# Optimization experiments

Hardware: AMD Instinct MI355X
Metric: run time of the kernel (lower is better)

Reference implementation:

```python
import jax, jax.numpy as jnp
import numpy as np

B, L, D_IN, H, N, NL = 16, 5000, 12, 256, 32, 4  # N = d_state//2 complex modes


def layer_norm(x, g, b, eps=1e-5):
    m = x.mean(-1, keepdims=True)
    v = ((x - m) ** 2).mean(-1, keepdims=True)
    return (x - m) * jax.lax.rsqrt(v + eps) * g + b


def s4d_kernel(log_dt, logA_re, A_im, Cp, length):
    # S4D-style diagonal SSM kernel (ZOH discretization), conjugate-symmetric -> 2*real
    dt = jnp.exp(log_dt)                      # (H,)
    A = -jnp.exp(logA_re) + 1j * A_im         # (H, N)
    C = Cp[..., 0] + 1j * Cp[..., 1]          # (H, N)
    dtA = A * dt[:, None]                     # (H, N)
    Ct = C * (jnp.exp(dtA) - 1.0) / A         # (H, N)
    V = jnp.exp(dtA[:, :, None] * jnp.arange(length, dtype=log_dt.dtype))  # (H, N, L) Vandermonde
    return 2.0 * jnp.einsum('hn,hnl->hl', Ct, V).real  # (H, L)


def s4_block(u, log_dt, logA_re, A_im, Cp, D, W_glu, b_glu):
    # u: (B, L, H), transposed=False convention
    length = u.shape[1]
    K = s4d_kernel(log_dt, logA_re, A_im, Cp, length)     # (H, L)
    n_fft = 2 * length
    k_f = jnp.fft.rfft(K, n=n_fft)                        # (H, F)
    u_f = jnp.fft.rfft(u, n=n_fft, axis=1)                # (B, F, H)
    y = jnp.fft.irfft(u_f * k_f.T[None], n=n_fft, axis=1)[:, :length]  # causal conv
    y = y + u * D                                         # skip connection
    y = jax.nn.gelu(y)
    y = y @ W_glu + b_glu                                 # (B, L, 2H)
    return jax.nn.glu(y, axis=-1)                         # (B, L, H)


def setup_inputs() -> dict:
    key = jax.random.key(0)
    ks = jax.random.split(key, 8)
    dt_min, dt_max = 1e-3, 1e-1
    log_dt = np.log(dt_min) + jax.random.uniform(ks[2], (NL, H)) * (np.log(dt_max) - np.log(dt_min))
    A_im = jnp.broadcast_to(np.pi * jnp.arange(N, dtype=jnp.float32), (NL, H, N)).copy()
    return {
        'x': jax.random.normal(ks[0], (B, L, D_IN), jnp.float32),
        'W_in': jax.random.normal(ks[1], (D_IN, H), jnp.float32) / np.sqrt(D_IN),
        'b_in': jnp.zeros((H,), jnp.float32),
        'ln_g': jnp.ones((NL, H), jnp.float32),
        'ln_b': jnp.zeros((NL, H), jnp.float32),
        'log_dt': log_dt.astype(jnp.float32),
        'logA_re': jnp.full((NL, H, N), np.log(0.5), jnp.float32),
        'A_im': A_im,
        'Cp': jax.random.normal(ks[3], (NL, H, N, 2), jnp.float32) * (0.5 ** 0.5),
        'D': jax.random.normal(ks[4], (NL, H), jnp.float32),
        'W_glu': jax.random.normal(ks[5], (NL, H, 2 * H), jnp.float32) / np.sqrt(H),
        'b_glu': jnp.zeros((NL, 2 * H), jnp.float32),
        'fn_g': jnp.ones((H,), jnp.float32),
        'fn_b': jnp.zeros((H,), jnp.float32),
    }


def reference(x, W_in, b_in, ln_g, ln_b, log_dt, logA_re, A_im, Cp, D, W_glu, b_glu, fn_g, fn_b):
    x = x @ W_in + b_in  # (B, L, H)
    for i in range(NL):
        z = layer_norm(x, ln_g[i], ln_b[i])  # prenorm
        residual = z
        y = s4_block(z, log_dt[i], logA_re[i], A_im[i], Cp[i], D[i], W_glu[i], b_glu[i])
        x = y + residual  # dropout is identity in eval
    return layer_norm(x, fn_g, fn_b)
```

## Files before the change

### kernel.cpp

```cpp
#include <hip/hip_runtime.h>
#include <math.h>

#define BB 16
#define LL 5000
#define DIN 12
#define HH 256
#define NN 32
#define NLAYER 4
#define LC 128
#define NCH 40
#define TAIL 8
#define COLS (BB*NCH)
#define NROWS (BB*LL)
#define KU 192

typedef __attribute__((ext_vector_type(8))) _Float16 f16x8;
typedef __attribute__((ext_vector_type(4))) float f32x4;

__device__ __forceinline__ float fast_gelu(float a) {
  float z = fmaf(0.0713548163f * a, a * a, 1.5957691216f * a);
  float e = __expf(-z);
  return a * __builtin_amdgcn_rcpf(1.0f + e);
}

__device__ __forceinline__ unsigned pk2h(float a, float b) {
  union { _Float16 h[2]; unsigned u; } x;
  x.h[0] = (_Float16)a; x.h[1] = (_Float16)b;
  return x.u;
}

__device__ __forceinline__ float2 upk2(unsigned u) {
  union { unsigned u; _Float16 h[2]; } x;
  x.u = u;
  return make_float2((float)x.h[0], (float)x.h[1]);
}

__global__ __launch_bounds__(128) void paramT_kernel(
    const float* __restrict__ log_dt, const float* __restrict__ logA_re,
    const float* __restrict__ A_im, const float* __restrict__ Cp,
    const float* __restrict__ Dv, int l,
    _Float16* __restrict__ Tc, _Float16* __restrict__ V, float* __restrict__ WLc) {
  int h = blockIdx.x;
  int t = threadIdx.x;
  __shared__ float s_are[NN], s_aim[NN], s_cre[NN], s_cim[NN];
  __shared__ float s_K[128];
  if (t < NN) {
    int n = t;
    int idx = (l * HH + h) * NN + n;
    float dt = expf(log_dt[l * HH + h]);
    float Are = -expf(logA_re[idx]);
    float Aim = A_im[idx];
    float are = Are * dt, aim = Aim * dt;
    float e = expf(are);
    float wre = e * cosf(aim), wim = e * sinf(aim);
    float cr = Cp[2 * idx], ci = Cp[2 * idx + 1];
    float nre = wre - 1.0f, nim = wim;
    float tre = cr * nre - ci * nim;
    float tim = cr * nim + ci * nre;
    float inv = 1.0f / (Are * Are + Aim * Aim);
    s_are[n] = are; s_aim[n] = aim;
    s_cre[n] = 2.0f * (tre * Are + tim * Aim) * inv;
    s_cim[n] = 2.0f * (tim * Are - tre * Aim) * inv;
    float eL = expf(128.0f * are);
    float ang = 128.0f * aim;
    WLc[h * 64 + 2 * n] = eL * cosf(ang);
    WLc[h * 64 + 2 * n + 1] = eL * sinf(ang);
  }
  __syncthreads();
  {
    float ksum = 0.0f;
    unsigned* brow = (unsigned*)(Tc + ((size_t)h * 128 + t) * KU + 128);
    for (int n = 0; n < NN; n++) {
      float are = s_are[n], aim = s_aim[n];
      float cre = s_cre[n], cim = s_cim[n];
      float ft = (float)t;
      float E = expf(are * ft);
      float a = aim * ft;
      float wtre = E * cosf(a), wtim = E * sinf(a);
      ksum = fmaf(cre, wtre, ksum);
      ksum = fmaf(-cim, wtim, ksum);
      float ew = expf(are);
      float wre = ew * cosf(aim), wim = ew * sinf(aim);
      float wpre = wtre * wre - wtim * wim;
      float wpim = wtre * wim + wtim * wre;
      float bre = cre * wpre - cim * wpim;
      float bim = -(cre * wpim + cim * wpre);
      brow[n] = pk2h(bre, bim);
      float fk = (float)(127 - t);
      float E2 = expf(are * fk);
      float a2 = aim * fk;
      V[((size_t)h * 64 + 2 * n) * 128 + t] = (_Float16)(E2 * cosf(a2));
      V[((size_t)h * 64 + 2 * n + 1) * 128 + t] = (_Float16)(E2 * sinf(a2));
    }
    s_K[t] = ksum;
  }
  __syncthreads();
  float D = Dv[l * HH + h];
  unsigned* row = (unsigned*)(Tc + ((size_t)h * 128 + t) * KU);
  for (int q = 0; q < 64; q++) {
    float v0 = 0.0f, v1 = 0.0f;
    int d0 = t - 2 * q;
    int d1 = d0 - 1;
    if (d0 >= 0) v0 = s_K[d0] + (d0 == 0 ? D : 0.0f);
    if (d1 >= 0) v1 = s_K[d1] + (d1 == 0 ? D : 0.0f);
    row[q] = pk2h(v0, v1);
  }
}

__global__ __launch_bounds__(256) void wt_kernel(
    const float* __restrict__ W, _Float16* __restrict__ Wt) {
  int gid = blockIdx.x * 256 + threadIdx.x;
  int l = gid >> 9, col = gid & 511;
  const float* w = W + (size_t)l * HH * 512 + col;
  _Float16* o = Wt + (size_t)gid * HH;
  for (int k = 0; k < HH; k++) o[k] = (_Float16)(w[(size_t)k * 512]);
}

__global__ __launch_bounds__(256) void proj_kernel(
    const float* __restrict__ x, const float* __restrict__ Win,
    const float* __restrict__ bin, _Float16* __restrict__ X) {
  int tp = threadIdx.x & 127, rs = threadIdx.x >> 7;
  int h0 = 2 * tp;
  float w0[DIN], w1[DIN];
#pragma unroll
  for (int k = 0; k < DIN; k++) {
    w0[k] = Win[k * HH + h0];
    w1[k] = Win[k * HH + h0 + 1];
  }
  float b0 = bin[h0], b1 = bin[h0 + 1];
  for (int row = blockIdx.x * 2 + rs; row < NROWS; row += gridDim.x * 2) {
    float a0 = b0, a1 = b1;
#pragma unroll
    for (int k = 0; k < DIN; k++) {
      float xv = x[(size_t)row * DIN + k];
      a0 = fmaf(xv, w0[k], a0);
      a1 = fmaf(xv, w1[k], a1);
    }
    *(unsigned*)(X + (size_t)row * HH + h0) = pk2h(a0, a1);
  }
}

__global__ __launch_bounds__(256) void ln_kernel(
    const _Float16* __restrict__ in, float* __restrict__ out,
    const float* __restrict__ g, const float* __restrict__ b) {
  int wave = threadIdx.x >> 6, lane = threadIdx.x & 63;
  int row = blockIdx.x * 4 + wave;
  uint2 pv = *(const uint2*)(in + (size_t)row * HH + 4 * lane);
  float2 v01 = upk2(pv.x), v23 = upk2(pv.y);
  float s = v01.x + v01.y + v23.x + v23.y;
  float q = v01.x * v01.x + v01.y * v01.y + v23.x * v23.x + v23.y * v23.y;
#pragma unroll
  for (int m = 1; m < 64; m <<= 1) { s += __shfl_xor(s, m); q += __shfl_xor(q, m); }
  float mean = s * (1.0f / HH);
  float var = q * (1.0f / HH) - mean * mean;
  float rstd = rsqrtf(var + 1e-5f);
  float4 gg = ((const float4*)g)[lane];
  float4 bb = ((const float4*)b)[lane];
  float4 o;
  o.x = (v01.x - mean) * rstd * gg.x + bb.x;
  o.y = (v01.y - mean) * rstd * gg.y + bb.y;
  o.z = (v23.x - mean) * rstd * gg.z + bb.z;
  o.w = (v23.y - mean) * rstd * gg.w + bb.w;
  ((float4*)(out + (size_t)row * HH))[lane] = o;
}

__global__ __launch_bounds__(256) void lnU_kernel(
    _Float16* __restrict__ stream, _Float16* __restrict__ U,
    const float* __restrict__ g, const float* __restrict__ b) {
  __shared__ unsigned short Ut[128][260];
  int col = blockIdx.x;
  int bI = col / NCH, cI = col % NCH;
  int len = (cI == NCH - 1) ? TAIL : 128;
  int wave = threadIdx.x >> 6, lane = threadIdx.x & 63;
  if (len < 128) {
    for (int idx = threadIdx.x; idx < (128 - len) * 260; idx += 256) {
      int r = idx / 260;
      Ut[len + r][idx - r * 260] = 0;
    }
  }
  float4 gg = ((const float4*)g)[lane];
  float4 bv = ((const float4*)b)[lane];
  size_t base = ((size_t)bI * LL + (size_t)cI * 128) * HH;
  for (int it = 0; it < 32; it++) {
    int tau = it * 4 + wave;
    if (tau < len) {
      uint2 pv = *(const uint2*)(stream + base + (size_t)tau * HH + 4 * lane);
      float2 v01 = upk2(pv.x), v23 = upk2(pv.y);
      float s = v01.x + v01.y + v23.x + v23.y;
      float q = v01.x * v01.x + v01.y * v01.y + v23.x * v23.x + v23.y * v23.y;
#pragma unroll
      for (int m = 1; m < 64; m <<= 1) { s += __shfl_xor(s, m); q += __shfl_xor(q, m); }
      float mean = s * (1.0f / HH);
      float var = q * (1.0f / HH) - mean * mean;
      float rstd = rsqrtf(var + 1e-5f);
      float o0 = (v01.x - mean) * rstd * gg.x + bv.x;
      float o1 = (v01.y - mean) * rstd * gg.y + bv.y;
      float o2 = (v23.x - mean) * rstd * gg.z + bv.z;
      float o3 = (v23.y - mean) * rstd * gg.w + bv.w;
      uint2 p;
      p.x = pk2h(o0, o1);
      p.y = pk2h(o2, o3);
      *(uint2*)(stream + base + (size_t)tau * HH + 4 * lane) = p;
      *(uint2*)&Ut[tau][4 * lane] = p;
    }
  }
  __syncthreads();
  for (int rep = 0; rep < 8; rep++) {
    int linear = rep * 256 + threadIdx.x;
    int h = linear >> 3, ub = linear & 7;
    unsigned* dst = (unsigned*)(U + ((size_t)h * COLS + col) * KU);
#pragma unroll
    for (int s2 = 0; s2 < 8; s2++) {
      int u = ub + s2 * 8;
      unsigned val = (unsigned)Ut[2 * u][h] | ((unsigned)Ut[2 * u + 1][h] << 16);
      dst[u] = val;
    }
  }
}

__global__ __launch_bounds__(256) void gemmA_kernel(
    const _Float16* __restrict__ V, const _Float16* __restrict__ U,
    _Float16* __restrict__ P) {
  __shared__ _Float16 As[64 * 72];
  __shared__ _Float16 Bs[64 * 72];
  int h = blockIdx.x, c0 = blockIdx.y * 64;
  int t = threadIdx.x;
  int w = t >> 6, lane = t & 63, lr = lane & 15, quad = lane >> 4;
  int mh = w & 1, nh = w >> 1;
  f32x4 acc[2][2];
#pragma unroll
  for (int i = 0; i < 2; i++)
#pragma unroll
    for (int j = 0; j < 2; j++) acc[i][j] = (f32x4)(0.0f);

  for (int kt = 0; kt < 128; kt += 64) {
#pragma unroll
    for (int i = 0; i < 2; i++) {
      int idx = t + 256 * i;
      int m = idx >> 3, q = idx & 7;
      *(uint4*)&As[m * 72 + q * 8] =
          *(const uint4*)(V + ((size_t)h * 64 + m) * 128 + kt + q * 8);
      *(uint4*)&Bs[m * 72 + q * 8] =
          *(const uint4*)(U + ((size_t)h * COLS + c0 + m) * KU + kt + q * 8);
    }
    __syncthreads();
#pragma unroll
    for (int ks = 0; ks < 2; ks++) {
      f16x8 af[2], bf[2];
#pragma unroll
      for (int i = 0; i < 2; i++)
        af[i] = *(const f16x8*)&As[(mh * 32 + i * 16 + lr) * 72 + ks * 32 + quad * 8];
#pragma unroll
      for (int j = 0; j < 2; j++)
        bf[j] = *(const f16x8*)&Bs[(nh * 32 + j * 16 + lr) * 72 + ks * 32 + quad * 8];
#pragma unroll
      for (int i = 0; i < 2; i++)
#pragma unroll
        for (int j = 0; j < 2; j++)
          acc[i][j] = __builtin_amdgcn_mfma_f32_16x16x32_f16(af[i], bf[j], acc[i][j], 0, 0, 0);
    }
    __syncthreads();
  }
#pragma unroll
  for (int i = 0; i < 2; i++) {
#pragma unroll
    for (int j = 0; j < 2; j++) {
      int n2 = mh * 32 + i * 16 + quad * 4;
      int col = c0 + nh * 32 + j * 16 + lr;
      f32x4 a = acc[i][j];
      uint2 r;
      r.x = pk2h(a[0], a[1]);
      r.y = pk2h(a[2], a[3]);
      *(uint2*)(P + ((size_t)h * COLS + col) * 64 + n2) = r;
    }
  }
}

__global__ __launch_bounds__(256) void combine_kernel(
    const _Float16* __restrict__ P, _Float16* __restrict__ U,
    const float* __restrict__ WLc) {
  int h = blockIdx.x >> 1;
  int bh = blockIdx.x & 1;
  int n = threadIdx.x & 31;
  int b = bh * 8 + (threadIdx.x >> 5);
  float wre = WLc[h * 64 + 2 * n], wim = WLc[h * 64 + 2 * n + 1];
  const _Float16* p = P + ((size_t)h * COLS + (size_t)b * NCH) * 64 + 2 * n;
  _Float16* u = U + ((size_t)h * COLS + (size_t)b * NCH) * KU + 128 + 2 * n;
  float cre = 0.0f, cim = 0.0f;
#pragma unroll 4
  for (int c = 0; c < NCH; c++) {
    float2 v = upk2(*(const unsigned*)(p + (size_t)c * 64));
    *(unsigned*)(u + (size_t)c * KU) = pk2h(cre, cim);
    float nre = fmaf(wre, cre, v.x) - wim * cim;
    float nim = fmaf(wre, cim, v.y) + wim * cre;
    cre = nre; cim = nim;
  }
}

__global__ __launch_bounds__(256) void gemmC_kernel(
    const _Float16* __restrict__ Tc, const _Float16* __restrict__ U,
    _Float16* __restrict__ Yt) {
  __shared__ _Float16 As[128 * 72];
  __shared__ _Float16 Bs[64 * 72];
  int h = blockIdx.x, c0 = blockIdx.y * 64;
  int t = threadIdx.x;
  int w = t >> 6, lane = t & 63, lr = lane & 15, quad = lane >> 4;
  f32x4 acc[2][4];
#pragma unroll
  for (int i = 0; i < 2; i++)
#pragma unroll
    for (int j = 0; j < 4; j++) acc[i][j] = (f32x4)(0.0f);

  for (int kt = 0; kt < KU; kt += 64) {
#pragma unroll
    for (int i = 0; i < 4; i++) {
      int idx = t + 256 * i;
      int m = idx >> 3, q = idx & 7;
      *(uint4*)&As[m * 72 + q * 8] =
          *(const uint4*)(Tc + ((size_t)h * 128 + m) * KU + kt + q * 8);
    }
#pragma unroll
    for (int i = 0; i < 2; i++) {
      int idx = t + 256 * i;
      int jj = idx >> 3, q = idx & 7;
      *(uint4*)&Bs[jj * 72 + q * 8] =
          *(const uint4*)(U + ((size_t)h * COLS + c0 + jj) * KU + kt + q * 8);
    }
    __syncthreads();
#pragma unroll
    for (int ks = 0; ks < 2; ks++) {
      f16x8 af[2], bf[4];
#pragma unroll
      for (int i = 0; i < 2; i++)
        af[i] = *(const f16x8*)&As[(w * 32 + i * 16 + lr) * 72 + ks * 32 + quad * 8];
#pragma unroll
      for (int j = 0; j < 4; j++)
        bf[j] = *(const f16x8*)&Bs[(j * 16 + lr) * 72 + ks * 32 + quad * 8];
#pragma unroll
      for (int i = 0; i < 2; i++)
#pragma unroll
        for (int j = 0; j < 4; j++)
          acc[i][j] = __builtin_amdgcn_mfma_f32_16x16x32_f16(af[i], bf[j], acc[i][j], 0, 0, 0);
    }
    __syncthreads();
  }
#pragma unroll
  for (int i = 0; i < 2; i++) {
#pragma unroll
    for (int j = 0; j < 4; j++) {
      int tb = w * 32 + i * 16 + quad * 4;
      int col = c0 + j * 16 + lr;
      f32x4 a = acc[i][j];
      uint2 r;
      r.x = pk2h(fast_gelu(a[0]), fast_gelu(a[1]));
      r.y = pk2h(fast_gelu(a[2]), fast_gelu(a[3]));
      *(uint2*)(Yt + ((size_t)h * COLS + col) * 128 + tb) = r;
    }
  }
}

__global__ __launch_bounds__(256) void gemm_glu_mfma(
    const _Float16* __restrict__ Yt, const _Float16* __restrict__ Wt,
    const float* __restrict__ bg, _Float16* __restrict__ Xio) {
  __shared__ uint4 smemq[2304];
  _Float16* As = (_Float16*)smemq;
  _Float16* Bs = (_Float16*)smemq + 128 * 64;
  float* gl = (float*)smemq;
  int t = threadIdx.x;
  int col = blockIdx.x;
  int bI = col / NCH, pt = col % NCH;
  int len = (pt == NCH - 1) ? TAIL : 128;
  size_t row0 = (size_t)bI * LL + (size_t)pt * 128;
  int c0 = blockIdx.y * 64;
  int w = t >> 6, lane = t & 63;
  int lr = lane & 15, quad = lane >> 4;
  int rh = w & 1, ch = w >> 1;
  int oct = lane & 15, hq = lane >> 4;
  f32x4 acc[4][4];
#pragma unroll
  for (int i = 0; i < 4; i++)
#pragma unroll
    for (int j = 0; j < 4; j++) acc[i][j] = (f32x4)(0.0f);

  int jb[4] = {ch * 32, ch * 32 + 16, 64 + ch * 32, 80 + ch * 32};

  for (int kt = 0; kt < HH; kt += 64) {
#pragma unroll
    for (int p = 0; p < 4; p++) {
      int hl = p * 16 + w * 4 + hq;
      uint4 v = *(const uint4*)(Yt + ((size_t)(kt + hl) * COLS + col) * 128 + oct * 8);
      uint4 pv;
      pv.x = __shfl_xor((int)v.x, 16);
      pv.y = __shfl_xor((int)v.y, 16);
      pv.z = __shfl_xor((int)v.z, 16);
      pv.w = __shfl_xor((int)v.w, 16);
      if ((hq & 1) == 0) {
        const unsigned short* sv = (const unsigned short*)&v;
        const unsigned short* qv = (const unsigned short*)&pv;
        int h8 = hl >> 3;
        int hb2 = (hl & 7) * 2;
#pragma unroll
        for (int j = 0; j < 8; j++) {
          int tt = oct * 8 + j;
          int so = h8 ^ (tt & 7) ^ ((tt >> 3) & 7);
          *(unsigned*)((char*)As + tt * 128 + so * 16 + hb2) =
              (unsigned)sv[j] | ((unsigned)qv[j] << 16);
        }
      }
    }
#pragma unroll
    for (int i = 0; i < 4; i++) {
      int idx = t + 256 * i;
      int jj = idx >> 3, q = idx & 7;
      int colw = (jj < 64) ? (c0 + jj) : (192 + c0 + jj);
      *(uint4*)&Bs[jj * 72 + q * 8] =
          *(const uint4*)(Wt + (size_t)colw * HH + kt + q * 8);
    }
    __syncthreads();
#pragma unroll
    for (int ks = 0; ks < 2; ks++) {
      f16x8 af[4], bf[4];
#pragma unroll
      for (int i = 0; i < 4; i++) {
        int tt = rh * 64 + i * 16 + lr;
        int so = (ks * 4 + quad) ^ (tt & 7) ^ ((tt >> 3) & 7);
        af[i] = *(const f16x8*)((const char*)As + tt * 128 + so * 16);
      }
#pragma unroll
      for (int j = 0; j < 4; j++)
        bf[j] = *(const f16x8*)&Bs[(jb[j] + lr) * 72 + ks * 32 + quad * 8];
#pragma unroll
      for (int i = 0; i < 4; i++)
#pragma unroll
        for (int j = 0; j < 4; j++)
          acc[i][j] = __builtin_amdgcn_mfma_f32_16x16x32_f16(af[i], bf[j], acc[i][j], 0, 0, 0);
    }
    __syncthreads();
  }

#pragma unroll
  for (int i = 0; i < 4; i++) {
#pragma unroll
    for (int r = 0; r < 4; r++) {
      int rowl = rh * 64 + i * 16 + quad * 4 + r;
#pragma unroll
      for (int jp = 0; jp < 2; jp++) {
        int hl = ch * 32 + jp * 16 + lr;
        int h = c0 + hl;
        float g1 = acc[i][jp][r] + bg[h];
        float g2 = acc[i][jp + 2][r] + bg[256 + h];
        float sig = __builtin_amdgcn_rcpf(1.0f + __expf(-g2));
        gl[rowl * 68 + hl] = g1 * sig;
      }
    }
  }
  __syncthreads();

#pragma unroll
  for (int rep = 0; rep < 4; rep++) {
    int lin = rep * 256 + t;
    int rowl = lin >> 3, hc = lin & 7;
    if (rowl < len) {
      size_t row = row0 + rowl;
      int hb = c0 + hc * 8;
      uint4 zv = *(const uint4*)(Xio + row * HH + hb);
      float2 z01 = upk2(zv.x), z23 = upk2(zv.y), z45 = upk2(zv.z), z67 = upk2(zv.w);
      const float* gp = &gl[rowl * 68 + hc * 8];
      uint4 r;
      r.x = pk2h(gp[0] + z01.x, gp[1] + z01.y);
      r.y = pk2h(gp[2] + z23.x, gp[3] + z23.y);
      r.z = pk2h(gp[4] + z45.x, gp[5] + z45.y);
      r.w = pk2h(gp[6] + z67.x, gp[7] + z67.y);
      *(uint4*)(Xio + row * HH + hb) = r;
    }
  }
}

extern "C" void kernel_launch(void* const* d_in, const int* in_sizes, int n_in,
                              void* d_out, int out_size, void* d_ws, size_t ws_size,
                              hipStream_t stream) {
  const float* x      = (const float*)d_in[0];
  const float* Win    = (const float*)d_in[1];
  const float* bin    = (const float*)d_in[2];
  const float* ln_g   = (const float*)d_in[3];
  const float* ln_b   = (const float*)d_in[4];
  const float* log_dt = (const float*)d_in[5];
  const float* logA   = (const float*)d_in[6];
  const float* A_im   = (const float*)d_in[7];
  const float* Cp     = (const float*)d_in[8];
  const float* Dv     = (const float*)d_in[9];
  const float* Wglu   = (const float*)d_in[10];
  const float* bglu   = (const float*)d_in[11];
  const float* fn_g   = (const float*)d_in[12];
  const float* fn_b   = (const float*)d_in[13];
  float* out = (float*)d_out;
  float* ws = (float*)d_ws;

  _Float16* Xs = (_Float16*)ws;
  float* Pf = ws + (size_t)NROWS * HH;
  _Float16* Tc = (_Float16*)(Pf + (size_t)HH * COLS * 64);
  _Float16* V  = Tc + (size_t)HH * 128 * KU;
  _Float16* U  = V + (size_t)HH * 64 * 128;
  _Float16* Wt = U + (size_t)HH * COLS * KU;
  float* WLc = (float*)(Wt + (size_t)NLAYER * 512 * HH);
  _Float16* P16 = (_Float16*)Pf;
  _Float16* Yt  = (_Float16*)Pf;

  wt_kernel<<<(NLAYER * 512) / 256, 256, 0, stream>>>(Wglu, Wt);
  proj_kernel<<<2048, 256, 0, stream>>>(x, Win, bin, Xs);

  for (int l = 0; l < NLAYER; l++) {
    paramT_kernel<<<HH, 128, 0, stream>>>(log_dt, logA, A_im, Cp, Dv, l, Tc, V, WLc);
    lnU_kernel<<<COLS, 256, 0, stream>>>(Xs, U, ln_g + l * HH, ln_b + l * HH);
    gemmA_kernel<<<dim3(HH, COLS / 64), 256, 0, stream>>>(V, U, P16);
    combine_kernel<<<HH * 2, 256, 0, stream>>>(P16, U, WLc);
    gemmC_kernel<<<dim3(HH, COLS / 64), 256, 0, stream>>>(Tc, U, Yt);
    gemm_glu_mfma<<<dim3(COLS, 4), 256, 0, stream>>>(
        Yt, Wt + (size_t)l * 512 * HH, bglu + (size_t)l * 2 * HH, Xs);
  }
  ln_kernel<<<NROWS / 4, 256, 0, stream>>>(Xs, out, fn_g, fn_b);
}
```

Measured before the change: 1.019 ms.

## Widen GEMM column tiles, halve lnU shared memory, rework GLU transpose stores

The two chunk GEMMs (gemmA and gemmC) now process 128 columns per block instead of 64, which doubles accumulator registers and reuses each A tile across more columns. lnU handles the chunk in two 64-row halves, so its shared-memory buffer is half the size and more blocks can be resident. The GLU kernel's LDS transpose now has every lane write four packed words with a changed swizzle, replacing a path where half the lanes wrote eight words each. The larger tiles give fewer blocks (1280 instead of 2560) and more register pressure in exchange for less redundant loading.

```diff
diff --git a/kernel.cpp b/kernel.cpp
--- a/kernel.cpp
+++ b/kernel.cpp
@@ -167,53 +167,58 @@
 __global__ __launch_bounds__(256) void lnU_kernel(
     _Float16* __restrict__ stream, _Float16* __restrict__ U,
     const float* __restrict__ g, const float* __restrict__ b) {
-  __shared__ unsigned short Ut[128][260];
+  __shared__ unsigned short Ut[64][260];
   int col = blockIdx.x;
   int bI = col / NCH, cI = col % NCH;
   int len = (cI == NCH - 1) ? TAIL : 128;
   int wave = threadIdx.x >> 6, lane = threadIdx.x & 63;
-  if (len < 128) {
-    for (int idx = threadIdx.x; idx < (128 - len) * 260; idx += 256) {
-      int r = idx / 260;
-      Ut[len + r][idx - r * 260] = 0;
-    }
-  }
   float4 gg = ((const float4*)g)[lane];
   float4 bv = ((const float4*)b)[lane];
   size_t base = ((size_t)bI * LL + (size_t)cI * 128) * HH;
-  for (int it = 0; it < 32; it++) {
-    int tau = it * 4 + wave;
-    if (tau < len) {
-      uint2 pv = *(const uint2*)(stream + base + (size_t)tau * HH + 4 * lane);
-      float2 v01 = upk2(pv.x), v23 = upk2(pv.y);
-      float s = v01.x + v01.y + v23.x + v23.y;
-      float q = v01.x * v01.x + v01.y * v01.y + v23.x * v23.x + v23.y * v23.y;
-#pragma unroll
-      for (int m = 1; m < 64; m <<= 1) { s += __shfl_xor(s, m); q += __shfl_xor(q, m); }
-      float mean = s * (1.0f / HH);
-      float var = q * (1.0f / HH) - mean * mean;
-      float rstd = rsqrtf(var + 1e-5f);
-      float o0 = (v01.x - mean) * rstd * gg.x + bv.x;
-      float o1 = (v01.y - mean) * rstd * gg.y + bv.y;
-      float o2 = (v23.x - mean) * rstd * gg.z + bv.z;
-      float o3 = (v23.y - mean) * rstd * gg.w + bv.w;
-      uint2 p;
-      p.x = pk2h(o0, o1);
-      p.y = pk2h(o2, o3);
-      *(uint2*)(stream + base + (size_t)tau * HH + 4 * lane) = p;
-      *(uint2*)&Ut[tau][4 * lane] = p;
-    }
-  }
-  __syncthreads();
-  for (int rep = 0; rep < 8; rep++) {
-    int linear = rep * 256 + threadIdx.x;
-    int h = linear >> 3, ub = linear & 7;
-    unsigned* dst = (unsigned*)(U + ((size_t)h * COLS + col) * KU);
-#pragma unroll
-    for (int s2 = 0; s2 < 8; s2++) {
-      int u = ub + s2 * 8;
-      unsigned val = (unsigned)Ut[2 * u][h] | ((unsigned)Ut[2 * u + 1][h] << 16);
-      dst[u] = val;
+#pragma unroll
+  for (int half = 0; half < 2; half++) {
+    if (half) __syncthreads();
+    int t0 = half * 64;
+    int lenh = len - t0;
+    lenh = lenh < 0 ? 0 : (lenh > 64 ? 64 : lenh);
+    for (int idx = threadIdx.x; idx < (64 - lenh) * 260; idx += 256) {
+      int r = idx / 260;
+      Ut[lenh + r][idx - r * 260] = 0;
+    }
+    for (int it = 0; it < 16; it++) {
+      int tl = it * 4 + wave;
+      if (tl < lenh) {
+        int tau = t0 + tl;
+        uint2 pv = *(const uint2*)(stream + base + (size_t)tau * HH + 4 * lane);
+        float2 v01 = upk2(pv.x), v23 = upk2(pv.y);
+        float s = v01.x + v01.y + v23.x + v23.y;
+        float q = v01.x * v01.x + v01.y * v01.y + v23.x * v23.x + v23.y * v23.y;
+#pragma unroll
+        for (int m = 1; m < 64; m <<= 1) { s += __shfl_xor(s, m); q += __shfl_xor(q, m); }
+        float mean = s * (1.0f / HH);
+        float var = q * (1.0f / HH) - mean * mean;
+        float rstd = rsqrtf(var + 1e-5f);
+        float o0 = (v01.x - mean) * rstd * gg.x + bv.x;
+        float o1 = (v01.y - mean) * rstd * gg.y + bv.y;
+        float o2 = (v23.x - mean) * rstd * gg.z + bv.z;
+        float o3 = (v23.y - mean) * rstd * gg.w + bv.w;
+        uint2 p;
+        p.x = pk2h(o0, o1);
+        p.y = pk2h(o2, o3);
+        *(uint2*)(stream + base + (size_t)tau * HH + 4 * lane) = p;
+        *(uint2*)&Ut[tl][4 * lane] = p;
+      }
+    }
+    __syncthreads();
+    for (int rep = 0; rep < 8; rep++) {
+      int linear = rep * 256 + threadIdx.x;
+      int h = linear >> 3, ub = linear & 7;
+      unsigned* dst = (unsigned*)(U + ((size_t)h * COLS + col) * KU) + half * 32;
+#pragma unroll
+      for (int s2 = 0; s2 < 4; s2++) {
+        int u = ub + s2 * 8;
+        dst[u] = (unsigned)Ut[2 * u][h] | ((unsigned)Ut[2 * u + 1][h] << 16);
+      }
     }
   }
 }
@@ -222,16 +227,16 @@
     const _Float16* __restrict__ V, const _Float16* __restrict__ U,
     _Float16* __restrict__ P) {
   __shared__ _Float16 As[64 * 72];
-  __shared__ _Float16 Bs[64 * 72];
-  int h = blockIdx.x, c0 = blockIdx.y * 64;
+  __shared__ _Float16 Bs[128 * 72];
+  int h = blockIdx.x, c0 = blockIdx.y * 128;
   int t = threadIdx.x;
   int w = t >> 6, lane = t & 63, lr = lane & 15, quad = lane >> 4;
   int mh = w & 1, nh = w >> 1;
-  f32x4 acc[2][2];
+  f32x4 acc[2][4];
 #pragma unroll
   for (int i = 0; i < 2; i++)
 #pragma unroll
-    for (int j = 0; j < 2; j++) acc[i][j] = (f32x4)(0.0f);
+    for (int j = 0; j < 4; j++) acc[i][j] = (f32x4)(0.0f);
 
   for (int kt = 0; kt < 128; kt += 64) {
 #pragma unroll
@@ -240,23 +245,28 @@
       int m = idx >> 3, q = idx & 7;
       *(uint4*)&As[m * 72 + q * 8] =
           *(const uint4*)(V + ((size_t)h * 64 + m) * 128 + kt + q * 8);
-      *(uint4*)&Bs[m * 72 + q * 8] =
-          *(const uint4*)(U + ((size_t)h * COLS + c0 + m) * KU + kt + q * 8);
+    }
+#pragma unroll
+    for (int i = 0; i < 4; i++) {
+      int idx = t + 256 * i;
+      int jj = idx >> 3, q = idx & 7;
+      *(uint4*)&Bs[jj * 72 + q * 8] =
+          *(const uint4*)(U + ((size_t)h * COLS + c0 + jj) * KU + kt + q * 8);
     }
     __syncthreads();
 #pragma unroll
     for (int ks = 0; ks < 2; ks++) {
-      f16x8 af[2], bf[2];
+      f16x8 af[2], bf[4];
 #pragma unroll
       for (int i = 0; i < 2; i++)
         af[i] = *(const f16x8*)&As[(mh * 32 + i * 16 + lr) * 72 + ks * 32 + quad * 8];
 #pragma unroll
-      for (int j = 0; j < 2; j++)
-        bf[j] = *(const f16x8*)&Bs[(nh * 32 + j * 16 + lr) * 72 + ks * 32 + quad * 8];
+      for (int j = 0; j < 4; j++)
+        bf[j] = *(const f16x8*)&Bs[(nh * 64 + j * 16 + lr) * 72 + ks * 32 + quad * 8];
 #pragma unroll
       for (int i = 0; i < 2; i++)
 #pragma unroll
-        for (int j = 0; j < 2; j++)
+        for (int j = 0; j < 4; j++)
           acc[i][j] = __builtin_amdgcn_mfma_f32_16x16x32_f16(af[i], bf[j], acc[i][j], 0, 0, 0);
     }
     __syncthreads();
@@ -264,14 +274,14 @@
 #pragma unroll
   for (int i = 0; i < 2; i++) {
 #pragma unroll
-    for (int j = 0; j < 2; j++) {
+    for (int j = 0; j < 4; j++) {
       int n2 = mh * 32 + i * 16 + quad * 4;
-      int col = c0 + nh * 32 + j * 16 + lr;
+      int colx = c0 + nh * 64 + j * 16 + lr;
       f32x4 a = acc[i][j];
       uint2 r;
       r.x = pk2h(a[0], a[1]);
       r.y = pk2h(a[2], a[3]);
-      *(uint2*)(P + ((size_t)h * COLS + col) * 64 + n2) = r;
+      *(uint2*)(P + ((size_t)h * COLS + colx) * 64 + n2) = r;
     }
   }
 }
@@ -301,15 +311,15 @@
     const _Float16* __restrict__ Tc, const _Float16* __restrict__ U,
     _Float16* __restrict__ Yt) {
   __shared__ _Float16 As[128 * 72];
-  __shared__ _Float16 Bs[64 * 72];
-  int h = blockIdx.x, c0 = blockIdx.y * 64;
+  __shared__ _Float16 Bs[128 * 72];
+  int h = blockIdx.x, c0 = blockIdx.y * 128;
   int t = threadIdx.x;
   int w = t >> 6, lane = t & 63, lr = lane & 15, quad = lane >> 4;
-  f32x4 acc[2][4];
+  f32x4 acc[2][8];
 #pragma unroll
   for (int i = 0; i < 2; i++)
 #pragma unroll
-    for (int j = 0; j < 4; j++) acc[i][j] = (f32x4)(0.0f);
+    for (int j = 0; j < 8; j++) acc[i][j] = (f32x4)(0.0f);
 
   for (int kt = 0; kt < KU; kt += 64) {
 #pragma unroll
@@ -320,7 +330,7 @@
           *(const uint4*)(Tc + ((size_t)h * 128 + m) * KU + kt + q * 8);
     }
 #pragma unroll
-    for (int i = 0; i < 2; i++) {
+    for (int i = 0; i < 4; i++) {
       int idx = t + 256 * i;
       int jj = idx >> 3, q = idx & 7;
       *(uint4*)&Bs[jj * 72 + q * 8] =
@@ -329,17 +339,17 @@
     __syncthreads();
 #pragma unroll
     for (int ks = 0; ks < 2; ks++) {
-      f16x8 af[2], bf[4];
+      f16x8 af[2], bf[8];
 #pragma unroll
       for (int i = 0; i < 2; i++)
         af[i] = *(const f16x8*)&As[(w * 32 + i * 16 + lr) * 72 + ks * 32 + quad * 8];
 #pragma unroll
-      for (int j = 0; j < 4; j++)
+      for (int j = 0; j < 8; j++)
         bf[j] = *(const f16x8*)&Bs[(j * 16 + lr) * 72 + ks * 32 + quad * 8];
 #pragma unroll
       for (int i = 0; i < 2; i++)
 #pragma unroll
-        for (int j = 0; j < 4; j++)
+        for (int j = 0; j < 8; j++)
           acc[i][j] = __builtin_amdgcn_mfma_f32_16x16x32_f16(af[i], bf[j], acc[i][j], 0, 0, 0);
     }
     __syncthreads();
@@ -347,14 +357,14 @@
 #pragma unroll
   for (int i = 0; i < 2; i++) {
 #pragma unroll
-    for (int j = 0; j < 4; j++) {
+    for (int j = 0; j < 8; j++) {
       int tb = w * 32 + i * 16 + quad * 4;
-      int col = c0 + j * 16 + lr;
+      int colx = c0 + j * 16 + lr;
       f32x4 a = acc[i][j];
       uint2 r;
       r.x = pk2h(fast_gelu(a[0]), fast_gelu(a[1]));
       r.y = pk2h(fast_gelu(a[2]), fast_gelu(a[3]));
-      *(uint2*)(Yt + ((size_t)h * COLS + col) * 128 + tb) = r;
+      *(uint2*)(Yt + ((size_t)h * COLS + colx) * 128 + tb) = r;
     }
   }
 }
@@ -376,6 +386,9 @@
   int lr = lane & 15, quad = lane >> 4;
   int rh = w & 1, ch = w >> 1;
   int oct = lane & 15, hq = lane >> 4;
+  int godd = hq & 1;
+  int jbase = godd * 4;
+  int goct = (oct + (oct >> 3)) & 7;
   f32x4 acc[4][4];
 #pragma unroll
   for (int i = 0; i < 4; i++)
@@ -394,19 +407,20 @@
       pv.y = __shfl_xor((int)v.y, 16);
       pv.z = __shfl_xor((int)v.z, 16);
       pv.w = __shfl_xor((int)v.w, 16);
-      if ((hq & 1) == 0) {
-        const unsigned short* sv = (const unsigned short*)&v;
-        const unsigned short* qv = (const unsigned short*)&pv;
-        int h8 = hl >> 3;
-        int hb2 = (hl & 7) * 2;
-#pragma unroll
-        for (int j = 0; j < 8; j++) {
-          int tt = oct * 8 + j;
-          int so = h8 ^ (tt & 7) ^ ((tt >> 3) & 7);
-          *(unsigned*)((char*)As + tt * 128 + so * 16 + hb2) =
-              (unsigned)sv[j] | ((unsigned)qv[j] << 16);
-        }
-      }
+      unsigned a0 = godd ? pv.z : v.x;
+      unsigned a1 = godd ? pv.w : v.y;
+      unsigned b0 = godd ? v.z : pv.x;
+      unsigned b1 = godd ? v.w : pv.y;
+      unsigned p0 = (a0 & 0xffffu) | (b0 << 16);
+      unsigned p1 = (a0 >> 16) | (b0 & 0xffff0000u);
+      unsigned p2 = (a1 & 0xffffu) | (b1 << 16);
+      unsigned p3 = (a1 >> 16) | (b1 & 0xffff0000u);
+      int soc = (hl >> 3) ^ goct;
+      char* basep = (char*)As + oct * 1024 + (hl & 6) * 2;
+      { int j = jbase;     *(unsigned*)(basep + j * 128 + ((soc ^ j) * 16)) = p0; }
+      { int j = jbase + 1; *(unsigned*)(basep + j * 128 + ((soc ^ j) * 16)) = p1; }
+      { int j = jbase + 2; *(unsigned*)(basep + j * 128 + ((soc ^ j) * 16)) = p2; }
+      { int j = jbase + 3; *(unsigned*)(basep + j * 128 + ((soc ^ j) * 16)) = p3; }
     }
 #pragma unroll
     for (int i = 0; i < 4; i++) {
@@ -423,7 +437,8 @@
 #pragma unroll
       for (int i = 0; i < 4; i++) {
         int tt = rh * 64 + i * 16 + lr;
-        int so = (ks * 4 + quad) ^ (tt & 7) ^ ((tt >> 3) & 7);
+        int ttg = tt >> 3;
+        int so = (ks * 4 + quad) ^ (tt & 7) ^ ((ttg + (ttg >> 3)) & 7);
         af[i] = *(const f16x8*)((const char*)As + tt * 128 + so * 16);
       }
 #pragma unroll
@@ -512,9 +527,9 @@
   for (int l = 0; l < NLAYER; l++) {
     paramT_kernel<<<HH, 128, 0, stream>>>(log_dt, logA, A_im, Cp, Dv, l, Tc, V, WLc);
     lnU_kernel<<<COLS, 256, 0, stream>>>(Xs, U, ln_g + l * HH, ln_b + l * HH);
-    gemmA_kernel<<<dim3(HH, COLS / 64), 256, 0, stream>>>(V, U, P16);
+    gemmA_kernel<<<dim3(HH, COLS / 128), 256, 0, stream>>>(V, U, P16);
     combine_kernel<<<HH * 2, 256, 0, stream>>>(P16, U, WLc);
-    gemmC_kernel<<<dim3(HH, COLS / 64), 256, 0, stream>>>(Tc, U, Yt);
+    gemmC_kernel<<<dim3(HH, COLS / 128), 256, 0, stream>>>(Tc, U, Yt);
     gemm_glu_mfma<<<dim3(COLS, 4), 256, 0, stream>>>(
         Yt, Wt + (size_t)l * 512 * HH, bglu + (size_t)l * 2 * HH, Xs);
   }
```

After: 901.9 us. -11.5%, faster.
